# Kernel optimization log

Hardware: AMD Instinct MI355X
Metric: run time of the kernel (lower is better)

## Reference

```python
import jax, jax.numpy as jnp
import numpy as np

INF = 1000.0
K = 128  # number of classes; ys drawn from [0, K) so unique(ys) == arange(K)
EPS = 1e-12  # guards sqrt gradient at zero distance


def _pairwise_sqdist(a, b):
    # squared euclidean distances between rows of a [N,D] and b [M,D] -> [N,M]
    a2 = jnp.sum(a * a, axis=-1, keepdims=True)
    b2 = jnp.sum(b * b, axis=-1)
    return jnp.maximum(a2 + b2[None, :] - 2.0 * (a @ b.T), 0.0)


def setup_inputs() -> dict:
    key = jax.random.key(0)
    k1, k2 = jax.random.split(key)
    Ns, D, Nq = 4096, 1024, 4096
    xs = jax.random.normal(k1, (Ns, D), dtype=jnp.float32)
    ys = jax.random.randint(k2, (Ns,), 0, K)
    pos = jnp.arange(Nq)
    xq = xs[pos]
    yq = ys[pos]
    return {"xq": xq, "yq": yq, "xs": xs, "ys": ys, "pos": pos}


def reference(xq, yq, xs, ys, pos):
    T = 1.0
    Nq = xq.shape[0]
    ind = jnp.arange(Nq)

    # ---- no-grad bookkeeping ----
    classes = jnp.arange(K)
    one_hot = ys[:, None] == classes[None, :]            # [Ns, K]
    class_count = jnp.sum(one_hot, axis=0)               # [K]
    yq_new = ys[pos]                                     # class id of each query (== nonzero of one_hot[pos])
    class_mask = yq[:, None] == ys[None, :]              # [Nq, Ns]
    idx = jnp.sum(class_mask, axis=-1) > 1               # queries with >1 same-class support samples
    # drop query's own support entry from the mask when the class has other samples
    class_mask = class_mask.at[ind, pos].set(class_mask[ind, pos] & ~idx)

    # ---- prototypes ----
    mus = one_hot.astype(xs.dtype).T @ xs                # [K, D] per-class sums
    M = mus[yq_new] - xq                                 # leave-one-out sums  [Nq, D]
    C = (class_count[yq_new] - 1).astype(xs.dtype)
    proto = M / jnp.clip(C, 0.1)[:, None]                # leave-one-out prototypes [Nq, D]
    proto_n = mus / jnp.clip(class_count.astype(xs.dtype), 0.1)[:, None]  # [K, D]

    # ---- denominator logits (plain p=2 cdist, per torch branch for l2_dist) ----
    d_pos = jnp.sqrt(jnp.sum((xq - proto) ** 2, axis=-1) + EPS)   # diag of cdist(xq, proto)
    logit_den = -jnp.sqrt(_pairwise_sqdist(xq, proto_n) + EPS)    # [Nq, K]
    logit_den = logit_den.at[ind, yq_new].set(-d_pos)
    neg_logit = jax.nn.logsumexp(logit_den, axis=1, keepdims=True)  # [Nq, 1]

    # ---- numerator logits: l2_dist(xq, xs) / T = -cdist^2 / 2 / T ----
    logit = -_pairwise_sqdist(xq, xs) / 2.0 / T          # [Nq, Ns]
    logit = logit.at[ind, pos].set(0.0)                  # logit[ind, pos] *= 0
    logit = logit.at[ind, pos].add(jnp.where(idx, -INF, 0.0))
    cm = class_mask.astype(logit.dtype)
    pos_logit = jnp.sum(logit * cm, axis=-1) / jnp.sum(cm, axis=-1)

    loss = jnp.mean(neg_logit - pos_logit[:, None])
    return loss
```

## Files before the change

kernel.cpp:

```cpp
#include <hip/hip_runtime.h>
#include <hip/hip_bf16.h>


#define KCLS 128
#define QB 16
#define BK 64

typedef __attribute__((ext_vector_type(8))) short short8;
typedef __attribute__((ext_vector_type(4))) float f32x4;

__device__ __forceinline__ short f2bs(float f) {
    __hip_bfloat16 h = __float2bfloat16(f);
    short s; __builtin_memcpy(&s, &h, 2); return s;
}

__global__ __launch_bounds__(256) void class_stats2(
    const float* __restrict__ xs, const int* __restrict__ ys,
    int Ns, int D,
    short* __restrict__ protoC,
    float* __restrict__ S2part,
    float* __restrict__ mu2part,
    int* __restrict__ cntArr, float* __restrict__ out)
{
    const int c = blockIdx.x >> 2;
    const int quarter = blockIdx.x & 3;
    const int t = threadIdx.x;
    const int dim = quarter * 256 + t;
    if (blockIdx.x == 0 && t == 0) out[0] = 0.f;
    __shared__ int list[4096];
    __shared__ int lcnt;
    __shared__ float red[256];
    if (t == 0) lcnt = 0;
    __syncthreads();
    for (int s = t; s < Ns; s += 256) {
        if (ys[s] == c) list[atomicAdd(&lcnt, 1)] = s;
    }
    __syncthreads();
    const int n = lcnt;
    float a = 0.f, s2p = 0.f;
    int r = 0;
    for (; r + 4 <= n; r += 4) {
        const float x0 = xs[(size_t)list[r]     * D + dim];
        const float x1 = xs[(size_t)list[r + 1] * D + dim];
        const float x2 = xs[(size_t)list[r + 2] * D + dim];
        const float x3 = xs[(size_t)list[r + 3] * D + dim];
        a += x0 + x1 + x2 + x3;
        s2p += x0 * x0 + x1 * x1 + x2 * x2 + x3 * x3;
    }
    for (; r < n; ++r) {
        const float x = xs[(size_t)list[r] * D + dim];
        a += x; s2p += x * x;
    }
    const float inv = 1.0f / fmaxf((float)n, 0.1f);
    protoC[(size_t)c * D + dim] = f2bs(a * inv);

    red[t] = a * a; __syncthreads();
    for (int o = 128; o > 0; o >>= 1) { if (t < o) red[t] += red[t + o]; __syncthreads(); }
    if (t == 0) mu2part[c * 4 + quarter] = red[0];
    __syncthreads();
    red[t] = s2p; __syncthreads();
    for (int o = 128; o > 0; o >>= 1) { if (t < o) red[t] += red[t + o]; __syncthreads(); }
    if (t == 0) {
        S2part[c * 4 + quarter] = red[0];
        if (quarter == 0) cntArr[c] = n;
    }
}

__global__ __launch_bounds__(256) void main_mfma(
    const float* __restrict__ xq, const int* __restrict__ yq,
    const int* __restrict__ ys, const int* __restrict__ posA,
    const short* __restrict__ protoC,
    const float* __restrict__ S2part, const float* __restrict__ mu2part,
    const int* __restrict__ cntArr, const float* __restrict__ xs,
    int Nq, int D, float invNq, float* __restrict__ out)
{
    const int t    = threadIdx.x;
    const int lane = t & 63;
    const int wave = t >> 6;
    const int quad = lane >> 4;
    const int l16  = lane & 15;
    const int qb0  = blockIdx.x * QB;

    __shared__ short Asb[2][QB * 72];
    __shared__ short Bsb[2][KCLS * 72];
    __shared__ float dotsS[QB * 132];
    __shared__ float pn2S[KCLS];
    __shared__ float mu2S[KCLS];
    __shared__ float S2S[KCLS];
    __shared__ int   cntIS[KCLS];
    __shared__ float q2S[QB], ownS[QB], diffS[QB];

    if (t < KCLS) {
        const int n = cntArr[t];
        const float cl = fmaxf((float)n, 0.1f);
        const float m2 = mu2part[t * 4] + mu2part[t * 4 + 1]
                       + mu2part[t * 4 + 2] + mu2part[t * 4 + 3];
        cntIS[t] = n;
        mu2S[t]  = m2;
        pn2S[t]  = m2 / (cl * cl);
        S2S[t]   = S2part[t * 4] + S2part[t * 4 + 1]
                 + S2part[t * 4 + 2] + S2part[t * 4 + 3];
    }

    const int sq = t >> 4;
    const int sk = (t & 15) * 4;
    const float* aRow = xq + (size_t)(qb0 + sq) * D;
    const float* sRow = xs + (size_t)posA[qb0 + sq] * D;
    const int bc  = t >> 3;
    const int bk8 = (t & 7) * 8;
    const short* bBase = protoC + (size_t)bc * D + bk8;
    const size_t bStride = (size_t)32 * D;

    f32x4 acc0 = {0.f, 0.f, 0.f, 0.f};
    f32x4 acc1 = {0.f, 0.f, 0.f, 0.f};
    float q2p = 0.f, ownp = 0.f;

    float4 av = *(const float4*)(aRow + sk);
    float4 sv = *(const float4*)(sRow + sk);
    int4 bv0 = *(const int4*)(bBase);
    int4 bv1 = *(const int4*)(bBase + bStride);
    int4 bv2 = *(const int4*)(bBase + 2 * bStride);
    int4 bv3 = *(const int4*)(bBase + 3 * bStride);

    const int aro = l16 * 72 + quad * 8;
    const int br0 = (32 * wave      + l16) * 72 + quad * 8;
    const int br1 = (32 * wave + 16 + l16) * 72 + quad * 8;

    for (int it = 0; it < 16; ++it) {
        short* Ab = Asb[it & 1];
        short* Bb = Bsb[it & 1];
        {
            short4 a16;
            a16.x = f2bs(av.x); a16.y = f2bs(av.y);
            a16.z = f2bs(av.z); a16.w = f2bs(av.w);
            *(short4*)(&Ab[sq * 72 + sk]) = a16;
        }
        *(int4*)(&Bb[bc * 72 + bk8]) = bv0;
        *(int4*)(&Bb[(bc + 32) * 72 + bk8]) = bv1;
        *(int4*)(&Bb[(bc + 64) * 72 + bk8]) = bv2;
        *(int4*)(&Bb[(bc + 96) * 72 + bk8]) = bv3;
        q2p += av.x * av.x + av.y * av.y + av.z * av.z + av.w * av.w;
        {
            const float dx = av.x - sv.x, dy = av.y - sv.y;
            const float dz = av.z - sv.z, dw = av.w - sv.w;
            ownp += dx * dx + dy * dy + dz * dz + dw * dw;
        }
        __syncthreads();
        if (it < 15) {
            const int kb = (it + 1) * BK;
            av = *(const float4*)(aRow + kb + sk);
            sv = *(const float4*)(sRow + kb + sk);
            bv0 = *(const int4*)(bBase + kb);
            bv1 = *(const int4*)(bBase + bStride + kb);
            bv2 = *(const int4*)(bBase + 2 * bStride + kb);
            bv3 = *(const int4*)(bBase + 3 * bStride + kb);
        }
        #pragma unroll
        for (int ks = 0; ks < BK; ks += 32) {
            const short8 a  = *(const short8*)(&Ab[aro + ks]);
            const short8 b0 = *(const short8*)(&Bb[br0 + ks]);
            const short8 b1 = *(const short8*)(&Bb[br1 + ks]);
            acc0 = __builtin_amdgcn_mfma_f32_16x16x32_bf16(a, b0, acc0, 0, 0, 0);
            acc1 = __builtin_amdgcn_mfma_f32_16x16x32_bf16(a, b1, acc1, 0, 0, 0);
        }
    }

    #pragma unroll
    for (int o = 1; o < 16; o <<= 1) {
        q2p  += __shfl_xor(q2p, o);
        ownp += __shfl_xor(ownp, o);
    }
    if ((t & 15) == 0) { q2S[sq] = q2p; ownS[sq] = ownp; }

    {
        const int cb = 32 * wave;
        #pragma unroll
        for (int r = 0; r < 4; ++r) {
            dotsS[(quad * 4 + r) * 132 + cb      + l16] = acc0[r];
            dotsS[(quad * 4 + r) * 132 + cb + 16 + l16] = acc1[r];
        }
    }
    __syncthreads();

    const int qg = t >> 4;
    const int cg = t & 15;
    const int qi = qb0 + qg;
    const float q2 = q2S[qg];

    const int p  = posA[qi];
    const int ci = ys[p];
    const int cnt_i = cntIS[ci];
    const float cnt_ci  = (float)cnt_i;
    const float clip_ci = fmaxf(cnt_ci, 0.1f);
    const float dotmu   = dotsS[qg * 132 + ci] * clip_ci;
    const float Ccl     = fmaxf(cnt_ci - 1.0f, 0.1f);
    const float dqM     = dotmu - q2;
    const float M2      = mu2S[ci] - 2.f * dotmu + q2;
    const float dpos2   = q2 - 2.f * dqM / Ccl + M2 / (Ccl * Ccl);
    const float d_pos   = sqrtf(fmaxf(dpos2, 0.f) + 1e-12f);

    float ld[8];
    float m = -3.0e38f;
    #pragma unroll
    for (int j = 0; j < 8; ++j) {
        const int c = cg * 8 + j;
        const float dot = dotsS[qg * 132 + c];
        const float sq_ = fmaxf(q2 + pn2S[c] - 2.f * dot, 0.f) + 1e-12f;
        float v = -sqrtf(sq_);
        if (c == ci) v = -d_pos;
        ld[j] = v;
        m = fmaxf(m, v);
    }
    #pragma unroll
    for (int o = 1; o < 16; o <<= 1) m = fmaxf(m, __shfl_xor(m, o));
    float se = 0.f;
    #pragma unroll
    for (int j = 0; j < 8; ++j) se += expf(ld[j] - m);
    #pragma unroll
    for (int o = 1; o < 16; o <<= 1) se += __shfl_xor(se, o);
    const float lse = m + logf(se);

    if (cg == 0) {
        const int cl = yq[qi];
        const int cntl_i = cntIS[cl];
        const float cntl = (float)cntl_i;
        const float dotmu_l = dotsS[qg * 132 + cl] * fmaxf(cntl, 0.1f);
        const float sum_sqd = cntl * q2 - 2.f * dotmu_l + S2S[cl];
        const bool m_own = (cl == ci);
        const bool idxq  = (cntl_i > 1);
        const float numer = -0.5f * (sum_sqd - (m_own ? ownS[qg] : 0.f));
        const float denom = cntl - ((m_own && idxq) ? 1.f : 0.f);
        diffS[qg] = lse - numer / denom;
    }
    __syncthreads();
    if (t == 0) {
        float ssum = 0.f;
        #pragma unroll
        for (int q = 0; q < QB; ++q) ssum += diffS[q];
        atomicAdd(out, ssum * invNq);
    }
}

extern "C" void kernel_launch(void* const* d_in, const int* in_sizes, int n_in,
                              void* d_out, int out_size, void* d_ws, size_t ws_size,
                              hipStream_t stream) {
    const float* xq  = (const float*)d_in[0];
    const int*   yq  = (const int*)d_in[1];
    const float* xs  = (const float*)d_in[2];
    const int*   ys  = (const int*)d_in[3];
    const int*   pos = (const int*)d_in[4];

    const int Nq = in_sizes[1];
    const int Ns = in_sizes[3];
    const int D  = in_sizes[0] / Nq;

    char* w = (char*)d_ws;
    short* protoC  = (short*)w;  w += (size_t)KCLS * D * sizeof(short);
    float* mu2part = (float*)w;  w += (size_t)KCLS * 4 * sizeof(float);
    float* S2part  = (float*)w;  w += (size_t)KCLS * 4 * sizeof(float);
    int*   cntA    = (int*)w;    w += KCLS * sizeof(int);

    float* out = (float*)d_out;

    class_stats2<<<KCLS * 4, 256, 0, stream>>>(xs, ys, Ns, D, protoC,
                                               S2part, mu2part, cntA, out);
    main_mfma<<<Nq / QB, 256, 0, stream>>>(xq, yq, ys, pos, protoC, S2part, mu2part,
                                           cntA, xs, Nq, D, 1.0f / (float)Nq, out);
}
```

Before: 102.2 us.

## Load MFMA operands directly from global memory, dropping LDS staging and barriers

Replaces the LDS double-buffered tiles for the query and prototype operands with direct per-lane global loads in MFMA fragment layout. Each wave now reads its own A fragment and B rows straight from global/L2 and issues the MFMAs, with no __syncthreads in the K loop. This removes the LDS write/read traffic and the block barriers. In exchange, all four waves redundantly load and convert the same A rows and q2/own partial sums, and global access becomes less coalesced (strided 32-byte chunks per lane).

```diff
diff --git a/kernel.cpp b/kernel.cpp
--- a/kernel.cpp
+++ b/kernel.cpp
@@ -4,7 +4,6 @@
 
 #define KCLS 128
 #define QB 16
-#define BK 64
 
 typedef __attribute__((ext_vector_type(8))) short short8;
 typedef __attribute__((ext_vector_type(4))) float f32x4;
@@ -81,8 +80,6 @@
     const int l16  = lane & 15;
     const int qb0  = blockIdx.x * QB;
 
-    __shared__ short Asb[2][QB * 72];
-    __shared__ short Bsb[2][KCLS * 72];
     __shared__ float dotsS[QB * 132];
     __shared__ float pn2S[KCLS];
     __shared__ float mu2S[KCLS];
@@ -102,75 +99,48 @@
                  + S2part[t * 4 + 2] + S2part[t * 4 + 3];
     }
 
-    const int sq = t >> 4;
-    const int sk = (t & 15) * 4;
-    const float* aRow = xq + (size_t)(qb0 + sq) * D;
-    const float* sRow = xs + (size_t)posA[qb0 + sq] * D;
-    const int bc  = t >> 3;
-    const int bk8 = (t & 7) * 8;
-    const short* bBase = protoC + (size_t)bc * D + bk8;
-    const size_t bStride = (size_t)32 * D;
+    const float* aRow = xq + (size_t)(qb0 + l16) * D + quad * 8;
+    const float* sRow = xs + (size_t)posA[qb0 + l16] * D + quad * 8;
+    const short* b0p  = protoC + (size_t)(32 * wave + l16) * D + quad * 8;
+    const short* b1p  = b0p + (size_t)16 * D;
 
     f32x4 acc0 = {0.f, 0.f, 0.f, 0.f};
     f32x4 acc1 = {0.f, 0.f, 0.f, 0.f};
     float q2p = 0.f, ownp = 0.f;
 
-    float4 av = *(const float4*)(aRow + sk);
-    float4 sv = *(const float4*)(sRow + sk);
-    int4 bv0 = *(const int4*)(bBase);
-    int4 bv1 = *(const int4*)(bBase + bStride);
-    int4 bv2 = *(const int4*)(bBase + 2 * bStride);
-    int4 bv3 = *(const int4*)(bBase + 3 * bStride);
-
-    const int aro = l16 * 72 + quad * 8;
-    const int br0 = (32 * wave      + l16) * 72 + quad * 8;
-    const int br1 = (32 * wave + 16 + l16) * 72 + quad * 8;
-
-    for (int it = 0; it < 16; ++it) {
-        short* Ab = Asb[it & 1];
-        short* Bb = Bsb[it & 1];
+    #pragma unroll 4
+    for (int kc = 0; kc < D; kc += 32) {
+        const float4 a0 = *(const float4*)(aRow + kc);
+        const float4 a1 = *(const float4*)(aRow + kc + 4);
+        const float4 s0 = *(const float4*)(sRow + kc);
+        const float4 s1 = *(const float4*)(sRow + kc + 4);
+        const short8 b0 = *(const short8*)(b0p + kc);
+        const short8 b1 = *(const short8*)(b1p + kc);
+
+        q2p += a0.x * a0.x + a0.y * a0.y + a0.z * a0.z + a0.w * a0.w
+             + a1.x * a1.x + a1.y * a1.y + a1.z * a1.z + a1.w * a1.w;
         {
-            short4 a16;
-            a16.x = f2bs(av.x); a16.y = f2bs(av.y);
-            a16.z = f2bs(av.z); a16.w = f2bs(av.w);
-            *(short4*)(&Ab[sq * 72 + sk]) = a16;
+            const float d0 = a0.x - s0.x, d1 = a0.y - s0.y;
+            const float d2 = a0.z - s0.z, d3 = a0.w - s0.w;
+            const float d4 = a1.x - s1.x, d5 = a1.y - s1.y;
+            const float d6 = a1.z - s1.z, d7 = a1.w - s1.w;
+            ownp += d0 * d0 + d1 * d1 + d2 * d2 + d3 * d3
+                  + d4 * d4 + d5 * d5 + d6 * d6 + d7 * d7;
         }
-        *(int4*)(&Bb[bc * 72 + bk8]) = bv0;
-        *(int4*)(&Bb[(bc + 32) * 72 + bk8]) = bv1;
-        *(int4*)(&Bb[(bc + 64) * 72 + bk8]) = bv2;
-        *(int4*)(&Bb[(bc + 96) * 72 + bk8]) = bv3;
-        q2p += av.x * av.x + av.y * av.y + av.z * av.z + av.w * av.w;
-        {
-            const float dx = av.x - sv.x, dy = av.y - sv.y;
-            const float dz = av.z - sv.z, dw = av.w - sv.w;
-            ownp += dx * dx + dy * dy + dz * dz + dw * dw;
-        }
-        __syncthreads();
-        if (it < 15) {
-            const int kb = (it + 1) * BK;
-            av = *(const float4*)(aRow + kb + sk);
-            sv = *(const float4*)(sRow + kb + sk);
-            bv0 = *(const int4*)(bBase + kb);
-            bv1 = *(const int4*)(bBase + bStride + kb);
-            bv2 = *(const int4*)(bBase + 2 * bStride + kb);
-            bv3 = *(const int4*)(bBase + 3 * bStride + kb);
-        }
-        #pragma unroll
-        for (int ks = 0; ks < BK; ks += 32) {
-            const short8 a  = *(const short8*)(&Ab[aro + ks]);
-            const short8 b0 = *(const short8*)(&Bb[br0 + ks]);
-            const short8 b1 = *(const short8*)(&Bb[br1 + ks]);
-            acc0 = __builtin_amdgcn_mfma_f32_16x16x32_bf16(a, b0, acc0, 0, 0, 0);
-            acc1 = __builtin_amdgcn_mfma_f32_16x16x32_bf16(a, b1, acc1, 0, 0, 0);
-        }
-    }
-
-    #pragma unroll
-    for (int o = 1; o < 16; o <<= 1) {
-        q2p  += __shfl_xor(q2p, o);
-        ownp += __shfl_xor(ownp, o);
-    }
-    if ((t & 15) == 0) { q2S[sq] = q2p; ownS[sq] = ownp; }
+
+        short8 a16;
+        a16[0] = f2bs(a0.x); a16[1] = f2bs(a0.y);
+        a16[2] = f2bs(a0.z); a16[3] = f2bs(a0.w);
+        a16[4] = f2bs(a1.x); a16[5] = f2bs(a1.y);
+        a16[6] = f2bs(a1.z); a16[7] = f2bs(a1.w);
+
+        acc0 = __builtin_amdgcn_mfma_f32_16x16x32_bf16(a16, b0, acc0, 0, 0, 0);
+        acc1 = __builtin_amdgcn_mfma_f32_16x16x32_bf16(a16, b1, acc1, 0, 0, 0);
+    }
+
+    q2p  += __shfl_xor(q2p, 16);  q2p  += __shfl_xor(q2p, 32);
+    ownp += __shfl_xor(ownp, 16); ownp += __shfl_xor(ownp, 32);
+    if (t < 16) { q2S[t] = q2p; ownS[t] = ownp; }
 
     {
         const int cb = 32 * wave;
```

Result: slower. 112.0 us (+9.6%).
